# Performance work log

Hardware: AMD Instinct MI355X
Metric: run time of the kernel (lower is better)

Reference implementation:

```python
import jax, jax.numpy as jnp
import numpy as np

B, IN, FS, S, H = 4096, 4096, 4096, 64, 512  # batch, input_size, first_size, shape_lstm, n_hidden
D = FS // S  # per-step feature for left/right (=64); up/down per-step feature = S (=64)


def _lstm_cell(x, h, c, Wih, Whh, bih, bhh):
    # standard torch LSTMCell gate order: i, f, g, o
    g = x @ Wih.T + bih + h @ Whh.T + bhh  # (B, 4H)
    i, f, gg, o = jnp.split(g, 4, axis=-1)
    c = jax.nn.sigmoid(f) * c + jax.nn.sigmoid(i) * jnp.tanh(gg)
    h = jax.nn.sigmoid(o) * jnp.tanh(c)
    return h, c


def setup_inputs() -> dict:
    key = jax.random.key(0)
    ks = jax.random.split(key, 20)
    def cell(k, d_in):
        k1, k2, k3, k4 = jax.random.split(k, 4)
        s = 1.0 / np.sqrt(H)
        return (jax.random.uniform(k1, (4 * H, d_in), jnp.float32, -s, s),
                jax.random.uniform(k2, (4 * H, H), jnp.float32, -s, s),
                jax.random.uniform(k3, (4 * H,), jnp.float32, -s, s),
                jax.random.uniform(k4, (4 * H,), jnp.float32, -s, s))
    Wih_l, Whh_l, bih_l, bhh_l = cell(ks[0], D)
    Wih_r, Whh_r, bih_r, bhh_r = cell(ks[1], D)
    Wih_d, Whh_d, bih_d, bhh_d = cell(ks[2], S)
    return {
        "x": jax.random.normal(ks[3], (B, IN), jnp.float32),
        "h0": jax.random.normal(ks[4], (4, B, H), jnp.float32),
        "c0": jax.random.normal(ks[5], (4, B, H), jnp.float32),
        "W1": jax.random.normal(ks[6], (FS, IN), jnp.float32) * (1.0 / np.sqrt(IN)),
        "b1": jnp.zeros((FS,), jnp.float32),
        "Wih_l": Wih_l, "Whh_l": Whh_l, "bih_l": bih_l, "bhh_l": bhh_l,
        "Wih_r": Wih_r, "Whh_r": Whh_r, "bih_r": bih_r, "bhh_r": bhh_r,
        "Wih_d": Wih_d, "Whh_d": Whh_d, "bih_d": bih_d, "bhh_d": bhh_d,
        "W3": jax.random.normal(ks[7], (10, 4 * H), jnp.float32) * (1.0 / np.sqrt(4 * H)),
        "b3": jnp.zeros((10,), jnp.float32),
    }


def reference(x, h0, c0, W1, b1, Wih_l, Whh_l, bih_l, bhh_l,
              Wih_r, Whh_r, bih_r, bhh_r, Wih_d, Whh_d, bih_d, bhh_d, W3, b3):
    feat = jax.nn.relu(x @ W1.T + b1)            # (B, FS); dropout=identity (eval)
    il = feat.reshape(B, S, D)
    x_left = jnp.transpose(il, (1, 0, 2))         # (S, B, D)
    x_right = x_left[::-1]
    x_up = jnp.transpose(il, (2, 0, 1))           # (D, B, S); loop uses first S steps
    x_down = x_up[::-1]

    def step(carry, xs):
        (hl, cl, hr, cr, hu, cu, hd, cd) = carry
        xl, xr, xu, xd = xs
        hl, cl = _lstm_cell(xl, hl, cl, Wih_l, Whh_l, bih_l, bhh_l)
        hr, cr = _lstm_cell(xr, hr, cr, Wih_r, Whh_r, bih_r, bhh_r)
        # original code uses the DOWN cell for both up and down directions
        hu, cu = _lstm_cell(xu, hu, cu, Wih_d, Whh_d, bih_d, bhh_d)
        hd, cd = _lstm_cell(xd, hd, cd, Wih_d, Whh_d, bih_d, bhh_d)
        return (hl, cl, hr, cr, hu, cu, hd, cd), None

    carry0 = (h0[0], c0[0], h0[1], c0[1], h0[2], c0[2], h0[3], c0[3])
    (hl, _, hr, _, hu, _, hd, _), _ = jax.lax.scan(
        step, carry0, (x_left[:S], x_right[:S], x_up[:S], x_down[:S]))
    out = jnp.concatenate([hl, hr, hu, hd], axis=1)  # (B, 4H)
    logits = out @ W3.T + b3
    return jax.nn.log_softmax(logits, axis=1)
```

## Files before the change

kernel.cpp:

```cpp
#include <hip/hip_runtime.h>
#include <cstddef>
#include <cstdint>

namespace {

constexpr int kB  = 4096;
constexpr int kIN = 4096;
constexpr int kFS = 4096;
constexpr int kS  = 64;
constexpr int kH  = 512;
constexpr int kNG = 2048;
constexpr int kKC = 576;
constexpr int kKTiles = kKC / 32;

typedef __bf16 bf16_t;
typedef __bf16 bfrag  __attribute__((ext_vector_type(8)));
typedef __bf16 bf16v4 __attribute__((ext_vector_type(4)));
typedef float  f32x4  __attribute__((ext_vector_type(4)));

__device__ __forceinline__ void gload16(const void* g, void* l) {
  __builtin_amdgcn_global_load_lds(
      (const __attribute__((address_space(1))) void*)g,
      (__attribute__((address_space(3))) void*)l, 16, 0, 0);
}

__device__ __forceinline__ float sigf(float x) { return 1.0f / (1.0f + __expf(-x)); }
__device__ __forceinline__ float tanh_fast(float x) {
  float e = __expf(2.0f * x);
  return 1.0f - 2.0f / (e + 1.0f);
}


__global__ __launch_bounds__(256) void f2b4_kernel(const float* __restrict__ in,
                                                   bf16_t* __restrict__ out, int n4) {
  int i = blockIdx.x * 256 + threadIdx.x;
  if (i >= n4) return;
  float4 v = reinterpret_cast<const float4*>(in)[i];
  bf16v4 o = {(bf16_t)v.x, (bf16_t)v.y, (bf16_t)v.z, (bf16_t)v.w};
  *reinterpret_cast<bf16v4*>(out + (size_t)i * 4) = o;
}

__global__ __launch_bounds__(256) void pack_wcat_kernel(
    const float* __restrict__ Wih_l, const float* __restrict__ Whh_l,
    const float* __restrict__ Wih_r, const float* __restrict__ Whh_r,
    const float* __restrict__ Wih_d, const float* __restrict__ Whh_d,
    bf16_t* __restrict__ wcat) {
  int idx = blockIdx.x * 256 + threadIdx.x;
  if (idx >= 3 * kNG * kKC) return;
  int m = idx / (kNG * kKC);
  int rem = idx - m * (kNG * kKC);
  int rr = rem / kKC;
  int k  = rem - rr * kKC;
  int u = rr >> 2, g = rr & 3;
  int orow = g * kH + u;
  const float* Wih = (m == 0) ? Wih_l : (m == 1) ? Wih_r : Wih_d;
  const float* Whh = (m == 0) ? Whh_l : (m == 1) ? Whh_r : Whh_d;
  float v = (k < 64) ? Wih[(size_t)orow * 64 + k] : Whh[(size_t)orow * 512 + (k - 64)];
  wcat[idx] = (bf16_t)v;
}

__global__ __launch_bounds__(256) void pack_bias_kernel(
    const float* __restrict__ bih_l, const float* __restrict__ bhh_l,
    const float* __restrict__ bih_r, const float* __restrict__ bhh_r,
    const float* __restrict__ bih_d, const float* __restrict__ bhh_d,
    float* __restrict__ biasc) {
  int idx = blockIdx.x * 256 + threadIdx.x;
  if (idx >= 3 * kNG) return;
  int m = idx / kNG;
  int rr = idx - m * kNG;
  int u = rr >> 2, g = rr & 3;
  int orow = g * kH + u;
  const float* bi = (m == 0) ? bih_l : (m == 1) ? bih_r : bih_d;
  const float* bh = (m == 0) ? bhh_l : (m == 1) ? bhh_r : bhh_d;
  biasc[idx] = bi[orow] + bh[orow];
}

__global__ __launch_bounds__(256) void pack_hc_kernel(const float* __restrict__ h0,
                                                      const float* __restrict__ c0,
                                                      bf16_t* __restrict__ hbuf0,
                                                      float* __restrict__ cbuf, int n) {
  int i = blockIdx.x * 256 + threadIdx.x;
  if (i >= n) return;
  hbuf0[i] = (bf16_t)h0[i];
  cbuf[i]  = c0[i];
}

__global__ __launch_bounds__(256) void transpose64_kernel(const bf16_t* __restrict__ feat,
                                                          bf16_t* __restrict__ featT) {
  __shared__ bf16_t tile[64][65];
  const int b = blockIdx.x;
  const bf16_t* src = feat + (size_t)b * kFS;
  bf16_t* dst = featT + (size_t)b * kFS;
  for (int i = threadIdx.x; i < 4096; i += 256) tile[i >> 6][i & 63] = src[i];
  __syncthreads();
  for (int i = threadIdx.x; i < 4096; i += 256) dst[i] = tile[i & 63][i >> 6];
}


__global__ __launch_bounds__(256, 4) void gemm_feat_kernel(
    const bf16_t* __restrict__ X, const bf16_t* __restrict__ W,
    const float* __restrict__ b1, bf16_t* __restrict__ feat) {
  __shared__ bf16_t As[128 * 32];
  __shared__ bf16_t Bs[128 * 32];
  const int t = threadIdx.x;
  const int bid = blockIdx.x;
  const int widx = (bid & 7) * 128 + (bid >> 3);
  const int bm = widx & 31, bn = widx >> 5;
  const int w = t >> 6, l = t & 63;
  const int wm = (w >> 1) * 64, wn = (w & 1) * 64;
  const int sr = t >> 2, sk = (t & 3) * 8;
  const int lr = l & 15, lk = (l >> 4) * 8;
  const int lrow4 = (l >> 4) * 4;

  f32x4 acc[4][4];
#pragma unroll
  for (int i = 0; i < 4; ++i)
#pragma unroll
    for (int j = 0; j < 4; ++j) acc[i][j] = (f32x4){0.f, 0.f, 0.f, 0.f};

  const bf16_t* ga = X + (size_t)(bm * 128 + sr) * kIN + sk;
  const bf16_t* gb = W + (size_t)(bn * 128 + sr) * kIN + sk;
  bf16_t* lA = As + w * 512;
  bf16_t* lB = Bs + w * 512;

  for (int kt = 0; kt < kIN / 32; ++kt) {
    gload16(ga, lA);
    gload16(ga + (size_t)64 * kIN, lA + 2048);
    gload16(gb, lB);
    gload16(gb + (size_t)64 * kIN, lB + 2048);
    ga += 32; gb += 32;
    __syncthreads();
    bfrag a[4], b[4];
#pragma unroll
    for (int mi = 0; mi < 4; ++mi)
      a[mi] = *reinterpret_cast<const bfrag*>(&As[(wm + mi * 16 + lr) * 32 + lk]);
#pragma unroll
    for (int ni = 0; ni < 4; ++ni)
      b[ni] = *reinterpret_cast<const bfrag*>(&Bs[(wn + ni * 16 + lr) * 32 + lk]);
#pragma unroll
    for (int mi = 0; mi < 4; ++mi)
#pragma unroll
      for (int ni = 0; ni < 4; ++ni)
        acc[mi][ni] = __builtin_amdgcn_mfma_f32_16x16x32_bf16(a[mi], b[ni], acc[mi][ni], 0, 0, 0);
    __syncthreads();
  }

#pragma unroll
  for (int ni = 0; ni < 4; ++ni) {
    const int col = bn * 128 + wn + ni * 16 + lr;
    const float bb = b1[col];
#pragma unroll
    for (int mi = 0; mi < 4; ++mi) {
#pragma unroll
      for (int r = 0; r < 4; ++r) {
        const int row = bm * 128 + wm + mi * 16 + lrow4 + r;
        float v = acc[mi][ni][r] + bb;
        feat[(size_t)row * kFS + col] = (bf16_t)fmaxf(v, 0.0f);
      }
    }
  }
}


__global__ __launch_bounds__(256, 4) void lstm_step_kernel(
    const bf16_t* __restrict__ feat, const bf16_t* __restrict__ featT,
    const bf16_t* __restrict__ wcat, const float* __restrict__ biasc,
    const bf16_t* __restrict__ hin, bf16_t* __restrict__ hout,
    float* __restrict__ cbuf, int s) {
  __shared__ __align__(16) unsigned char smem[32 * 132 * 4];
  bf16_t* As = (bf16_t*)smem;
  bf16_t* Bs = (bf16_t*)(smem + 8192);
  float*  Gs = (float*)smem;

  const int t = threadIdx.x;
  const int bid = blockIdx.x;
  const int widx = (bid & 7) * 256 + (bid >> 3);
  const int cell = widx >> 9;
  const int rwk  = widx & 511;
  const int bm = rwk >> 4, bn = rwk & 15;
  const int w = t >> 6, l = t & 63;
  const int wm = (w >> 1) * 64, wn = (w & 1) * 64;
  const int sr = t >> 2, sk = (t & 3) * 8;
  const int lr = l & 15, lk = (l >> 4) * 8;
  const int lrow4 = (l >> 4) * 4;

  const bf16_t* xsrc = (cell < 2) ? feat : featT;
  const int off = ((cell & 1) ? (63 - s) : s) * 64;
  const int mat = (cell < 2) ? cell : 2;
  const bf16_t* Wm = wcat + (size_t)mat * kNG * kKC;
  const bf16_t* hc = hin + (size_t)cell * kB * kH;

  f32x4 acc[4][4];
#pragma unroll
  for (int i = 0; i < 4; ++i)
#pragma unroll
    for (int j = 0; j < 4; ++j) acc[i][j] = (f32x4){0.f, 0.f, 0.f, 0.f};

  const bf16_t* gax = xsrc + (size_t)(bm * 128 + sr) * kFS + off + sk;
  const bf16_t* gah = hc + (size_t)(bm * 128 + sr) * kH + sk;
  const bf16_t* gb  = Wm + (size_t)(bn * 128 + sr) * kKC + sk;
  bf16_t* lA = As + w * 512;
  bf16_t* lB = Bs + w * 512;

  for (int kt = 0; kt < kKTiles; ++kt) {
    if (kt < 2) {
      const bf16_t* ga = gax + kt * 32;
      gload16(ga, lA);
      gload16(ga + (size_t)64 * kFS, lA + 2048);
    } else {
      const bf16_t* ga = gah + (kt - 2) * 32;
      gload16(ga, lA);
      gload16(ga + (size_t)64 * kH, lA + 2048);
    }
    gload16(gb, lB);
    gload16(gb + (size_t)64 * kKC, lB + 2048);
    gb += 32;
    __syncthreads();
    bfrag a[4], b[4];
#pragma unroll
    for (int mi = 0; mi < 4; ++mi)
      a[mi] = *reinterpret_cast<const bfrag*>(&As[(wm + mi * 16 + lr) * 32 + lk]);
#pragma unroll
    for (int ni = 0; ni < 4; ++ni)
      b[ni] = *reinterpret_cast<const bfrag*>(&Bs[(wn + ni * 16 + lr) * 32 + lk]);
#pragma unroll
    for (int mi = 0; mi < 4; ++mi)
#pragma unroll
      for (int ni = 0; ni < 4; ++ni)
        acc[mi][ni] = __builtin_amdgcn_mfma_f32_16x16x32_bf16(a[mi], b[ni], acc[mi][ni], 0, 0, 0);
    __syncthreads();
  }

  const float* biasn = biasc + mat * kNG + bn * 128;
#pragma unroll
  for (int pass = 0; pass < 4; ++pass) {
    const int half = pass >> 1;
    const int mlo  = (pass & 1) * 2;
    if ((w >> 1) == half) {
#pragma unroll
      for (int ni = 0; ni < 4; ++ni) {
        const int colL = wn + ni * 16 + lr;
        const float bb = biasn[colL];
#pragma unroll
        for (int mi = mlo; mi < mlo + 2; ++mi)
#pragma unroll
          for (int r = 0; r < 4; ++r)
            Gs[((mi - mlo) * 16 + lrow4 + r) * 132 + colL] = acc[mi][ni][r] + bb;
      }
    }
    __syncthreads();
#pragma unroll
    for (int it = 0; it < 4; ++it) {
      const int ci = it * 256 + t;
      const int rowL = ci >> 5;
      const int u = ci & 31;
      const float4 g4 = *reinterpret_cast<const float4*>(&Gs[rowL * 132 + u * 4]);
      const float iv = sigf(g4.x);
      const float fv = sigf(g4.y);
      const float gv = tanh_fast(g4.z);
      const float ov = sigf(g4.w);
      const int batch = bm * 128 + half * 64 + mlo * 16 + rowL;
      const int unit = bn * 32 + u;
      const size_t cidx = ((size_t)cell * kB + batch) * kH + unit;
      const float cn = fv * cbuf[cidx] + iv * gv;
      cbuf[cidx] = cn;
      hout[cidx] = (bf16_t)(ov * tanh_fast(cn));
    }
    __syncthreads();
  }
}


__global__ __launch_bounds__(256) void head_kernel(const bf16_t* __restrict__ hfin,
                                                   const float* __restrict__ W3,
                                                   const float* __restrict__ b3,
                                                   float* __restrict__ out) {
  const int b = blockIdx.x, t = threadIdx.x;
  float acc[10];
#pragma unroll
  for (int j = 0; j < 10; ++j) acc[j] = 0.f;
  for (int k = t; k < 2048; k += 256) {
    const int cell = k >> 9, u = k & 511;
    const float hv = (float)hfin[((size_t)cell * kB + b) * kH + u];
#pragma unroll
    for (int j = 0; j < 10; ++j) acc[j] += hv * W3[j * 2048 + k];
  }
  __shared__ float red[256];
  __shared__ float logits[10];
  for (int j = 0; j < 10; ++j) {
    red[t] = acc[j];
    __syncthreads();
    for (int o2 = 128; o2 > 0; o2 >>= 1) {
      if (t < o2) red[t] += red[t + o2];
      __syncthreads();
    }
    if (t == 0) logits[j] = red[0] + b3[j];
    __syncthreads();
  }
  if (t == 0) {
    float mx = logits[0];
    for (int j = 1; j < 10; ++j) mx = fmaxf(mx, logits[j]);
    float se = 0.f;
    for (int j = 0; j < 10; ++j) se += expf(logits[j] - mx);
    const float lse = mx + logf(se);
    for (int j = 0; j < 10; ++j) out[(size_t)b * 10 + j] = logits[j] - lse;
  }
}

}

extern "C" void kernel_launch(void* const* d_in, const int* in_sizes, int n_in,
                              void* d_out, int out_size, void* d_ws, size_t ws_size,
                              hipStream_t stream) {
  const float* x     = (const float*)d_in[0];
  const float* h0    = (const float*)d_in[1];
  const float* c0    = (const float*)d_in[2];
  const float* W1    = (const float*)d_in[3];
  const float* b1    = (const float*)d_in[4];
  const float* Wih_l = (const float*)d_in[5];
  const float* Whh_l = (const float*)d_in[6];
  const float* bih_l = (const float*)d_in[7];
  const float* bhh_l = (const float*)d_in[8];
  const float* Wih_r = (const float*)d_in[9];
  const float* Whh_r = (const float*)d_in[10];
  const float* bih_r = (const float*)d_in[11];
  const float* bhh_r = (const float*)d_in[12];
  const float* Wih_d = (const float*)d_in[13];
  const float* Whh_d = (const float*)d_in[14];
  const float* bih_d = (const float*)d_in[15];
  const float* bhh_d = (const float*)d_in[16];
  const float* W3    = (const float*)d_in[17];
  const float* b3    = (const float*)d_in[18];
  float* out = (float*)d_out;

  char* p = (char*)d_ws;
  auto take = [&](size_t bytes) {
    char* r = p;
    p += (bytes + 255) & ~(size_t)255;
    return r;
  };
  bf16_t* xb    = (bf16_t*)take((size_t)kB * kIN * 2);
  bf16_t* w1b   = (bf16_t*)take((size_t)kFS * kIN * 2);
  bf16_t* feat  = (bf16_t*)take((size_t)kB * kFS * 2);
  bf16_t* wcat  = (bf16_t*)take((size_t)3 * kNG * kKC * 2);
  float*  biasc = (float*)take((size_t)3 * kNG * 4);
  float*  cbuf  = (float*)take((size_t)4 * kB * kH * 4);
  bf16_t* featT = xb;
  bf16_t* hbuf  = w1b;
  const size_t HSZ = (size_t)4 * kB * kH;

  f2b4_kernel<<<(kB * kIN / 4) / 256, 256, 0, stream>>>(x, xb, kB * kIN / 4);
  f2b4_kernel<<<(kFS * kIN / 4) / 256, 256, 0, stream>>>(W1, w1b, kFS * kIN / 4);
  gemm_feat_kernel<<<dim3(1024), 256, 0, stream>>>(xb, w1b, b1, feat);
  transpose64_kernel<<<kB, 256, 0, stream>>>(feat, featT);
  pack_wcat_kernel<<<(3 * kNG * kKC + 255) / 256, 256, 0, stream>>>(
      Wih_l, Whh_l, Wih_r, Whh_r, Wih_d, Whh_d, wcat);
  pack_bias_kernel<<<(3 * kNG + 255) / 256, 256, 0, stream>>>(
      bih_l, bhh_l, bih_r, bhh_r, bih_d, bhh_d, biasc);
  pack_hc_kernel<<<(int)(HSZ / 256), 256, 0, stream>>>(h0, c0, hbuf, cbuf, (int)HSZ);

  for (int s = 0; s < 64; ++s) {
    lstm_step_kernel<<<dim3(2048), 256, 0, stream>>>(
        feat, featT, wcat, biasc,
        hbuf + (size_t)(s & 1) * HSZ, hbuf + (size_t)((s + 1) & 1) * HSZ, cbuf, s);
  }
  head_kernel<<<kB, 256, 0, stream>>>(hbuf, W3, b3, out);
}
```

Measured before the change: 4.359 ms.

## Use 256x128 tiles with triple-buffered async LDS pipeline in LSTM step GEMM

The per-step LSTM gate GEMM tile grows from 128x128 to 256x128 per block, halving the block count and the weight re-reads per batch row. The single-buffered load-sync-compute loop becomes a three-stage LDS ring. Loads are issued two k-tiles ahead, split into halves interleaved with the two MFMA halves, and synchronised with explicit vmcnt waits and raw barriers. It also adds an XOR swizzle on the LDS layout to cut bank conflicts and raises wave priority around MFMA bursts. The cost is more registers (32 accumulators) and 72KB of LDS per block, which lowers occupancy to 2 blocks per CU.

```diff
diff --git a/kernel.cpp b/kernel.cpp
--- a/kernel.cpp
+++ b/kernel.cpp
@@ -162,26 +162,25 @@
 }
 
 
-__global__ __launch_bounds__(256, 4) void lstm_step_kernel(
+__global__ __launch_bounds__(256, 2) void lstm_step_kernel(
     const bf16_t* __restrict__ feat, const bf16_t* __restrict__ featT,
     const bf16_t* __restrict__ wcat, const float* __restrict__ biasc,
     const bf16_t* __restrict__ hin, bf16_t* __restrict__ hout,
     float* __restrict__ cbuf, int s) {
-  __shared__ __align__(16) unsigned char smem[32 * 132 * 4];
-  bf16_t* As = (bf16_t*)smem;
-  bf16_t* Bs = (bf16_t*)(smem + 8192);
-  float*  Gs = (float*)smem;
+  __shared__ __align__(16) unsigned char smem[3 * 24576];
 
   const int t = threadIdx.x;
   const int bid = blockIdx.x;
-  const int widx = (bid & 7) * 256 + (bid >> 3);
-  const int cell = widx >> 9;
-  const int rwk  = widx & 511;
+  const int widx = (bid & 7) * 128 + (bid >> 3);
+  const int cell = widx >> 8;
+  const int rwk  = widx & 255;
   const int bm = rwk >> 4, bn = rwk & 15;
   const int w = t >> 6, l = t & 63;
-  const int wm = (w >> 1) * 64, wn = (w & 1) * 64;
-  const int sr = t >> 2, sk = (t & 3) * 8;
-  const int lr = l & 15, lk = (l >> 4) * 8;
+  const int wm = (w >> 1) * 128, wn = (w & 1) * 64;
+  const int sr = t >> 2;
+  const int skS = ((t & 3) ^ ((t >> 3) & 3)) * 8;
+  const int lr = l & 15;
+  const int lkS = (((l >> 4) ^ ((l >> 1) & 3)) * 8);
   const int lrow4 = (l >> 4) * 4;
 
   const bf16_t* xsrc = (cell < 2) ? feat : featT;
@@ -190,59 +189,110 @@
   const bf16_t* Wm = wcat + (size_t)mat * kNG * kKC;
   const bf16_t* hc = hin + (size_t)cell * kB * kH;
 
-  f32x4 acc[4][4];
-#pragma unroll
-  for (int i = 0; i < 4; ++i)
+  const bf16_t* gax2 = xsrc + (size_t)(bm * 256 + sr) * kFS + off + skS;
+  const bf16_t* gah2 = hc + (size_t)(bm * 256 + sr) * kH + skS;
+  const bf16_t* gbt  = Wm + (size_t)(bn * 128 + sr) * kKC + skS;
+
+  auto stageP1 = [&](int kt, int b) {
+    char* base = (char*)smem + b * 24576;
+    bf16_t* dA = (bf16_t*)base + w * 512;
+    bf16_t* dB = (bf16_t*)(base + 16384) + w * 512;
+    if (kt < 2) {
+      const bf16_t* g = gax2 + kt * 32;
+      gload16(g, dA);
+      gload16(g + (size_t)64 * kFS, dA + 2048);
+    } else {
+      const bf16_t* g = gah2 + (kt - 2) * 32;
+      gload16(g, dA);
+      gload16(g + (size_t)64 * kH, dA + 2048);
+    }
+    gload16(gbt + kt * 32, dB);
+  };
+  auto stageP2 = [&](int kt, int b) {
+    char* base = (char*)smem + b * 24576;
+    bf16_t* dA = (bf16_t*)base + 4096 + w * 512;
+    bf16_t* dB = (bf16_t*)(base + 16384) + 2048 + w * 512;
+    if (kt < 2) {
+      const bf16_t* g = gax2 + kt * 32 + (size_t)128 * kFS;
+      gload16(g, dA);
+      gload16(g + (size_t)64 * kFS, dA + 2048);
+    } else {
+      const bf16_t* g = gah2 + (kt - 2) * 32 + (size_t)128 * kH;
+      gload16(g, dA);
+      gload16(g + (size_t)64 * kH, dA + 2048);
+    }
+    gload16(gbt + kt * 32 + (size_t)64 * kKC, dB);
+  };
+
+  f32x4 acc[8][4];
+#pragma unroll
+  for (int i = 0; i < 8; ++i)
 #pragma unroll
     for (int j = 0; j < 4; ++j) acc[i][j] = (f32x4){0.f, 0.f, 0.f, 0.f};
 
-  const bf16_t* gax = xsrc + (size_t)(bm * 128 + sr) * kFS + off + sk;
-  const bf16_t* gah = hc + (size_t)(bm * 128 + sr) * kH + sk;
-  const bf16_t* gb  = Wm + (size_t)(bn * 128 + sr) * kKC + sk;
-  bf16_t* lA = As + w * 512;
-  bf16_t* lB = Bs + w * 512;
+  stageP1(0, 0); stageP2(0, 0);
+  stageP1(1, 1); stageP2(1, 1);
+  asm volatile("s_waitcnt vmcnt(6)" ::: "memory");
+  __builtin_amdgcn_sched_barrier(0);
+  __builtin_amdgcn_s_barrier();
 
   for (int kt = 0; kt < kKTiles; ++kt) {
-    if (kt < 2) {
-      const bf16_t* ga = gax + kt * 32;
-      gload16(ga, lA);
-      gload16(ga + (size_t)64 * kFS, lA + 2048);
-    } else {
-      const bf16_t* ga = gah + (kt - 2) * 32;
-      gload16(ga, lA);
-      gload16(ga + (size_t)64 * kH, lA + 2048);
-    }
-    gload16(gb, lB);
-    gload16(gb + (size_t)64 * kKC, lB + 2048);
-    gb += 32;
-    __syncthreads();
-    bfrag a[4], b[4];
+    const int cur = kt % 3;
+    const bf16_t* Asb = (const bf16_t*)(smem + cur * 24576);
+    const bf16_t* Bsb = (const bf16_t*)(smem + cur * 24576 + 16384);
+    const bool pf = (kt + 2 < kKTiles);
+    const int nb = (kt + 2) % 3;
+
+    if (pf) stageP1(kt + 2, nb);
+    bfrag af[8], bf[4];
 #pragma unroll
     for (int mi = 0; mi < 4; ++mi)
-      a[mi] = *reinterpret_cast<const bfrag*>(&As[(wm + mi * 16 + lr) * 32 + lk]);
+      af[mi] = *reinterpret_cast<const bfrag*>(&Asb[(wm + mi * 16 + lr) * 32 + lkS]);
 #pragma unroll
     for (int ni = 0; ni < 4; ++ni)
-      b[ni] = *reinterpret_cast<const bfrag*>(&Bs[(wn + ni * 16 + lr) * 32 + lk]);
+      bf[ni] = *reinterpret_cast<const bfrag*>(&Bsb[(wn + ni * 16 + lr) * 32 + lkS]);
+    __builtin_amdgcn_s_setprio(1);
 #pragma unroll
     for (int mi = 0; mi < 4; ++mi)
 #pragma unroll
       for (int ni = 0; ni < 4; ++ni)
-        acc[mi][ni] = __builtin_amdgcn_mfma_f32_16x16x32_bf16(a[mi], b[ni], acc[mi][ni], 0, 0, 0);
-    __syncthreads();
-  }
-
+        acc[mi][ni] = __builtin_amdgcn_mfma_f32_16x16x32_bf16(af[mi], bf[ni], acc[mi][ni], 0, 0, 0);
+    __builtin_amdgcn_s_setprio(0);
+    __builtin_amdgcn_s_barrier();
+
+    if (pf) stageP2(kt + 2, nb);
+#pragma unroll
+    for (int mi = 4; mi < 8; ++mi)
+      af[mi] = *reinterpret_cast<const bfrag*>(&Asb[(wm + mi * 16 + lr) * 32 + lkS]);
+    __builtin_amdgcn_s_setprio(1);
+#pragma unroll
+    for (int mi = 4; mi < 8; ++mi)
+#pragma unroll
+      for (int ni = 0; ni < 4; ++ni)
+        acc[mi][ni] = __builtin_amdgcn_mfma_f32_16x16x32_bf16(af[mi], bf[ni], acc[mi][ni], 0, 0, 0);
+    __builtin_amdgcn_s_setprio(0);
+
+    if (kt < kKTiles - 2) {
+      asm volatile("s_waitcnt vmcnt(6)" ::: "memory");
+    } else if (kt == kKTiles - 2) {
+      asm volatile("s_waitcnt vmcnt(0)" ::: "memory");
+    }
+    __builtin_amdgcn_sched_barrier(0);
+    __builtin_amdgcn_s_barrier();
+  }
+
+  float* Gs = (float*)smem;
   const float* biasn = biasc + mat * kNG + bn * 128;
 #pragma unroll
   for (int pass = 0; pass < 4; ++pass) {
-    const int half = pass >> 1;
-    const int mlo  = (pass & 1) * 2;
-    if ((w >> 1) == half) {
+    const int mlo = (pass & 1) * 4;
+    if ((w >> 1) == (pass >> 1)) {
 #pragma unroll
       for (int ni = 0; ni < 4; ++ni) {
         const int colL = wn + ni * 16 + lr;
         const float bb = biasn[colL];
 #pragma unroll
-        for (int mi = mlo; mi < mlo + 2; ++mi)
+        for (int mi = mlo; mi < mlo + 4; ++mi)
 #pragma unroll
           for (int r = 0; r < 4; ++r)
             Gs[((mi - mlo) * 16 + lrow4 + r) * 132 + colL] = acc[mi][ni][r] + bb;
@@ -250,7 +300,7 @@
     }
     __syncthreads();
 #pragma unroll
-    for (int it = 0; it < 4; ++it) {
+    for (int it = 0; it < 8; ++it) {
       const int ci = it * 256 + t;
       const int rowL = ci >> 5;
       const int u = ci & 31;
@@ -259,7 +309,7 @@
       const float fv = sigf(g4.y);
       const float gv = tanh_fast(g4.z);
       const float ov = sigf(g4.w);
-      const int batch = bm * 128 + half * 64 + mlo * 16 + rowL;
+      const int batch = bm * 256 + pass * 64 + rowL;
       const int unit = bn * 32 + u;
       const size_t cidx = ((size_t)cell * kB + batch) * kH + unit;
       const float cn = fv * cbuf[cidx] + iv * gv;
@@ -360,7 +410,7 @@
   pack_hc_kernel<<<(int)(HSZ / 256), 256, 0, stream>>>(h0, c0, hbuf, cbuf, (int)HSZ);
 
   for (int s = 0; s < 64; ++s) {
-    lstm_step_kernel<<<dim3(2048), 256, 0, stream>>>(
+    lstm_step_kernel<<<dim3(1024), 256, 0, stream>>>(
         feat, featT, wcat, biasc,
         hbuf + (size_t)(s & 1) * HSZ, hbuf + (size_t)((s + 1) & 1) * HSZ, cbuf, s);
   }
```

After: 4.564 ms. 4.7% more time.
